# Optimization experiments

Hardware: AMD Instinct MI355X
Metric: run time of the kernel (lower is better)

Reference implementation:

```python
import jax, jax.numpy as jnp
import numpy as np

N_NODES = 100000
DROPOUT_P = 0.2


def _gcn_conv(x, W, b, src, dst, n_nodes):
    # PyG GCNConv: h = x @ W; add self-loops; sym-norm deg^-1/2 aggregation; + bias
    h = x @ W  # [N, D_out]
    loops = jnp.arange(n_nodes, dtype=src.dtype)
    src_all = jnp.concatenate([src, loops])
    dst_all = jnp.concatenate([dst, loops])
    deg = jax.ops.segment_sum(jnp.ones_like(dst_all, dtype=h.dtype), dst_all,
                              num_segments=n_nodes)  # includes self-loops
    dinv = jnp.where(deg > 0, jax.lax.rsqrt(deg), 0.0)
    norm = dinv[src_all] * dinv[dst_all]  # [E+N]
    msg = h[src_all] * norm[:, None]      # gather + scale
    out = jax.ops.segment_sum(msg, dst_all, num_segments=n_nodes)  # scatter-add
    return out + b


def setup_inputs() -> dict:
    key = jax.random.key(0)
    k1, k2, k3, k4 = jax.random.split(key, 4)
    x = jax.random.normal(k1, (N_NODES, 128), dtype=jnp.float32)
    edge_index = jax.random.randint(k2, (2, 1600000), 0, N_NODES, dtype=jnp.int64)
    W1 = jax.random.normal(k3, (128, 64), dtype=jnp.float32) * (1.0 / np.sqrt(128))
    b1 = jnp.zeros((64,), dtype=jnp.float32)
    W2 = jax.random.normal(k4, (64, 32), dtype=jnp.float32) * (1.0 / np.sqrt(64))
    b2 = jnp.zeros((32,), dtype=jnp.float32)
    return {"x": x, "edge_index": edge_index, "W1": W1, "b1": b1, "W2": W2, "b2": b2}


def reference(x, edge_index, W1, b1, W2, b2):
    src, dst = edge_index[0], edge_index[1]
    h1 = _gcn_conv(x, W1, b1, src, dst, N_NODES)
    h1 = jax.nn.relu(h1)
    # F.dropout defaults to training=True -> apply inverted dropout with fixed key
    keep = jax.random.bernoulli(jax.random.key(42), 1.0 - DROPOUT_P, h1.shape)
    h1 = jnp.where(keep, h1 / (1.0 - DROPOUT_P), 0.0)
    h2 = _gcn_conv(h1, W2, b2, src, dst, N_NODES)
    return h2
```

## Files before the change

kernel.cpp:

```cpp
#include <hip/hip_runtime.h>
#include <stdint.h>

#define DIN 128
#define D1 64
#define D2 32
#define MAXDEG 48
#define BCAP 4608
#define CBLK 8192

__device__ __forceinline__ unsigned short f2bf(float v) {
  unsigned u = __float_as_uint(v);
  unsigned r = u + 0x7fffu + ((u >> 16) & 1u);
  return (unsigned short)(r >> 16);
}
__device__ __forceinline__ float bf2f(unsigned short b) {
  return __uint_as_float(((unsigned)b) << 16);
}

__device__ __forceinline__ float node_dinv(const int* __restrict__ deg, int n) {
  return (float)(1.0 / sqrt((double)(deg[n] + 1)));
}

__device__ __forceinline__ unsigned rotl32(unsigned x, int r) {
  return (x << r) | (x >> (32 - r));
}

__device__ __forceinline__ unsigned threefry_fold(unsigned ctr) {
  unsigned k0 = 0u, k1 = 42u;
  unsigned ks0 = k0, ks1 = k1, ks2 = k0 ^ k1 ^ 0x1BD11BDAu;
  unsigned x0 = 0u, x1 = ctr;
  x0 += ks0; x1 += ks1;
#define TF_ROUND(r) { x0 += x1; x1 = rotl32(x1, (r)); x1 ^= x0; }
  TF_ROUND(13) TF_ROUND(15) TF_ROUND(26) TF_ROUND(6)
  x0 += ks1; x1 += ks2 + 1u;
  TF_ROUND(17) TF_ROUND(29) TF_ROUND(16) TF_ROUND(24)
  x0 += ks2; x1 += ks0 + 2u;
  TF_ROUND(13) TF_ROUND(15) TF_ROUND(26) TF_ROUND(6)
  x0 += ks0; x1 += ks1 + 3u;
  TF_ROUND(17) TF_ROUND(29) TF_ROUND(16) TF_ROUND(24)
  x0 += ks1; x1 += ks2 + 4u;
  TF_ROUND(13) TF_ROUND(15) TF_ROUND(26) TF_ROUND(6)
  x0 += ks2; x1 += ks0 + 5u;
#undef TF_ROUND
  return x0 ^ x1;
}

__device__ __forceinline__ float dropout_scale(unsigned idx) {
  unsigned bits = threefry_fold(idx);
  float u = __uint_as_float((bits >> 9) | 0x3f800000u) - 1.0f;
  return (u < 0.8f) ? 1.25f : 0.0f;
}

__global__ __launch_bounds__(256) void bin_kernel(const int* __restrict__ src,
                                                  const int* __restrict__ dst,
                                                  int* __restrict__ cursor,
                                                  uint2* __restrict__ binned,
                                                  int E, int NBK) {
  __shared__ int cnt[512];
  __shared__ int cbase[512];
  const int tid = threadIdx.x;
  const int e0 = blockIdx.x * CBLK;

  for (int b = tid; b < NBK; b += 256) cnt[b] = 0;
  __syncthreads();

#pragma unroll 4
  for (int i = 0; i < CBLK / 256; i++) {
    int e = e0 + tid + 256 * i;
    if (e < E) atomicAdd(&cnt[dst[e] >> 8], 1);
  }
  __syncthreads();

  for (int b = tid; b < NBK; b += 256) {
    int c = cnt[b];
    if (c > 0) cbase[b] = b * BCAP + atomicAdd(&cursor[b], c);
    cnt[b] = 0;
  }
  __syncthreads();

#pragma unroll 4
  for (int i = 0; i < CBLK / 256; i++) {
    int e = e0 + tid + 256 * i;
    if (e < E) {
      int d = dst[e];
      int b = d >> 8;
      int rk = atomicAdd(&cnt[b], 1);
      int pos = cbase[b] + rk;
      if (pos - b * BCAP < BCAP)
        binned[pos] = make_uint2((unsigned)d, (unsigned)src[e]);
    }
  }
}

__global__ __launch_bounds__(256) void ellbuild_kernel(const uint2* __restrict__ binned,
                                                       const int* __restrict__ cursor,
                                                       int* __restrict__ deg,
                                                       int* __restrict__ ell, int N) {
  __shared__ int r[256];
  const int tid = threadIdx.x;
  const int b = blockIdx.x;
  const int nodebase = b << 8;
  r[tid] = 0;
  __syncthreads();

  int cnt = cursor[b];
  if (cnt > BCAP) cnt = BCAP;
  const uint2* seg = binned + (size_t)b * BCAP;
  for (int i = tid; i < cnt; i += 256) {
    uint2 p = seg[i];
    int local = (int)p.x - nodebase;
    int rk = atomicAdd(&r[local], 1);
    if (rk < MAXDEG) ell[(int)p.x * MAXDEG + rk] = (int)p.y;
  }
  __syncthreads();

  int node = nodebase + tid;
  if (node < N) deg[node] = r[tid];
}

__global__ __launch_bounds__(256) void gemm1_kernel(const float* __restrict__ x,
                                                    const float* __restrict__ W1,
                                                    const int* __restrict__ deg,
                                                    unsigned short* __restrict__ h1p, int N) {
  __shared__ float xT[32][65];
  __shared__ float Wl[32][D1];
  const int tid = threadIdx.x;
  const int rowbase = blockIdx.x * 64;
  const int tx = tid & 15;
  const int ty = tid >> 4;
  float acc[4][4];
#pragma unroll
  for (int i = 0; i < 4; i++)
#pragma unroll
    for (int j = 0; j < 4; j++) acc[i][j] = 0.f;

  for (int c4 = 0; c4 < 4; c4++) {
    const int k0 = c4 * 32;
#pragma unroll
    for (int i = 0; i < 2; i++) {
      int f = tid + 256 * i;
      int row = f >> 3;
      int kq = (f & 7) * 4;
      int gr = rowbase + row;
      float4 vv = make_float4(0.f, 0.f, 0.f, 0.f);
      if (gr < N) vv = *(const float4*)(x + (size_t)gr * DIN + k0 + kq);
      xT[kq + 0][row] = vv.x;
      xT[kq + 1][row] = vv.y;
      xT[kq + 2][row] = vv.z;
      xT[kq + 3][row] = vv.w;
    }
#pragma unroll
    for (int i = 0; i < 2; i++) {
      int f = tid + 256 * i;
      int k = f >> 4;
      int cc = (f & 15) * 4;
      *(float4*)&Wl[k][cc] = *(const float4*)(W1 + (size_t)(k0 + k) * D1 + cc);
    }
    __syncthreads();
#pragma unroll 4
    for (int k = 0; k < 32; k++) {
      float4 a = *(const float4*)&xT[k][4 * ty];
      float4 b = *(const float4*)&Wl[k][4 * tx];
      float av[4] = {a.x, a.y, a.z, a.w};
      float bv[4] = {b.x, b.y, b.z, b.w};
#pragma unroll
      for (int i = 0; i < 4; i++)
#pragma unroll
        for (int j = 0; j < 4; j++) acc[i][j] = fmaf(av[i], bv[j], acc[i][j]);
    }
    __syncthreads();
  }

#pragma unroll
  for (int i = 0; i < 4; i++) {
    int gr = rowbase + 4 * ty + i;
    if (gr < N) {
      float di = node_dinv(deg, gr);
      ushort4 o;
      o.x = f2bf(acc[i][0] * di);
      o.y = f2bf(acc[i][1] * di);
      o.z = f2bf(acc[i][2] * di);
      o.w = f2bf(acc[i][3] * di);
      *(ushort4*)(h1p + (size_t)gr * D1 + 4 * tx) = o;
    }
  }
}

__global__ __launch_bounds__(256) void agg1_kernel(const int* __restrict__ deg,
                                                   const int* __restrict__ ell,
                                                   const unsigned short* __restrict__ h1p,
                                                   const float* __restrict__ b1,
                                                   float* __restrict__ h1d, int N) {
  const int wslot = __builtin_amdgcn_readfirstlane(threadIdx.x >> 6);
  const int d = blockIdx.x * 4 + wslot;
  const int f = threadIdx.x & 63;
  const int cnt = min(deg[d], MAXDEG);
  const int base = d * MAXDEG;
  float acc = bf2f(h1p[(size_t)d * D1 + f]);
  int j = 0;
  for (; j + 7 < cnt; j += 8) {
    int s[8];
#pragma unroll
    for (int i = 0; i < 8; i++) s[i] = ell[base + j + i];
    unsigned short a[8];
#pragma unroll
    for (int i = 0; i < 8; i++) a[i] = h1p[(size_t)s[i] * D1 + f];
#pragma unroll
    for (int i = 0; i < 8; i++) acc += bf2f(a[i]);
  }
  for (; j < cnt; ++j) acc += bf2f(h1p[(size_t)ell[base + j] * D1 + f]);
  float di = node_dinv(deg, d);
  float v = fmaf(di, acc, b1[f]);
  v = fmaxf(v, 0.0f);
  v *= dropout_scale((unsigned)(d * D1 + f));
  h1d[(size_t)d * D1 + f] = v;
}

__global__ __launch_bounds__(256) void gemm2_kernel(const float* __restrict__ h1d,
                                                    const float* __restrict__ W2,
                                                    const int* __restrict__ deg,
                                                    unsigned short* __restrict__ h2p, int N) {
  __shared__ float hT[D1][129];
  __shared__ float Wl[D1][D2];
  const int tid = threadIdx.x;
  const int rowbase = blockIdx.x * 128;

#pragma unroll
  for (int i = 0; i < 8; i++) {
    int f = tid + 256 * i;
    int row = f >> 4;
    int kq = (f & 15) * 4;
    int gr = rowbase + row;
    float4 v = make_float4(0.f, 0.f, 0.f, 0.f);
    if (gr < N) v = *(const float4*)(h1d + (size_t)gr * D1 + kq);
    hT[kq + 0][row] = v.x;
    hT[kq + 1][row] = v.y;
    hT[kq + 2][row] = v.z;
    hT[kq + 3][row] = v.w;
  }
#pragma unroll
  for (int i = 0; i < 2; i++) {
    int f = tid + 256 * i;
    int k = f >> 3;
    int c = (f & 7) * 4;
    *(float4*)&Wl[k][c] = *(const float4*)(W2 + (size_t)k * D2 + c);
  }
  __syncthreads();

  const int tx = tid & 7;
  const int ty = tid >> 3;
  float acc[4][4];
#pragma unroll
  for (int i = 0; i < 4; i++)
#pragma unroll
    for (int j = 0; j < 4; j++) acc[i][j] = 0.f;

#pragma unroll 4
  for (int k = 0; k < D1; k++) {
    float4 a = *(const float4*)&hT[k][4 * ty];
    float4 b = *(const float4*)&Wl[k][4 * tx];
    float av[4] = {a.x, a.y, a.z, a.w};
    float bv[4] = {b.x, b.y, b.z, b.w};
#pragma unroll
    for (int i = 0; i < 4; i++)
#pragma unroll
      for (int j = 0; j < 4; j++) acc[i][j] = fmaf(av[i], bv[j], acc[i][j]);
  }

#pragma unroll
  for (int i = 0; i < 4; i++) {
    int gr = rowbase + 4 * ty + i;
    if (gr < N) {
      float di = node_dinv(deg, gr);
      ushort4 o;
      o.x = f2bf(acc[i][0] * di);
      o.y = f2bf(acc[i][1] * di);
      o.z = f2bf(acc[i][2] * di);
      o.w = f2bf(acc[i][3] * di);
      *(ushort4*)(h2p + (size_t)gr * D2 + 4 * tx) = o;
    }
  }
}

__global__ __launch_bounds__(256) void agg2_kernel(const int* __restrict__ deg,
                                                   const int* __restrict__ ell,
                                                   const unsigned short* __restrict__ h2p,
                                                   const float* __restrict__ b2,
                                                   float* __restrict__ out, int N) {
  const int wslot = __builtin_amdgcn_readfirstlane(threadIdx.x >> 6);
  const int d = blockIdx.x * 4 + wslot;
  const int lane = threadIdx.x & 63;
  const int f = lane & 31;
  const int h = lane >> 5;
  const int cnt = min(deg[d], MAXDEG);
  const int base = d * MAXDEG;
  float acc = (h == 0) ? bf2f(h2p[(size_t)d * D2 + f]) : 0.0f;
  int j = h;
  for (; j + 6 < cnt; j += 8) {
    int s0 = ell[base + j], s1 = ell[base + j + 2];
    int s2 = ell[base + j + 4], s3 = ell[base + j + 6];
    unsigned short a0 = h2p[(size_t)s0 * D2 + f];
    unsigned short a1 = h2p[(size_t)s1 * D2 + f];
    unsigned short a2 = h2p[(size_t)s2 * D2 + f];
    unsigned short a3 = h2p[(size_t)s3 * D2 + f];
    acc += bf2f(a0); acc += bf2f(a1); acc += bf2f(a2); acc += bf2f(a3);
  }
  for (; j < cnt; j += 2) acc += bf2f(h2p[(size_t)ell[base + j] * D2 + f]);
  acc += __shfl_down(acc, 32, 64);
  if (h == 0) {
    out[(size_t)d * D2 + f] = fmaf(node_dinv(deg, d), acc, b2[f]);
  }
}

extern "C" void kernel_launch(void* const* d_in, const int* in_sizes, int n_in,
                              void* d_out, int out_size, void* d_ws, size_t ws_size,
                              hipStream_t stream) {
  const float* x  = (const float*)d_in[0];
  const int*   ei = (const int*)d_in[1];
  const float* W1 = (const float*)d_in[2];
  const float* b1 = (const float*)d_in[3];
  const float* W2 = (const float*)d_in[4];
  const float* b2 = (const float*)d_in[5];
  const int N = in_sizes[0] / DIN;
  const int E = in_sizes[1] / 2;
  const int NBK = (N + 255) >> 8;
  const int* src = ei;
  const int* dst = ei + E;
  float* out = (float*)d_out;

  char* ws = (char*)d_ws;
  size_t off = 0;
  auto alloc = [&](size_t bytes) -> char* {
    char* p = ws + off;
    off += (bytes + 255) / 256 * 256;
    return p;
  };
  unsigned short* h1p = (unsigned short*)alloc((size_t)N * D1 * 2);
  float*          h1d = (float*)alloc((size_t)N * D1 * 4);
  int*            ell = (int*)alloc((size_t)N * MAXDEG * 4);
  int*            deg = (int*)alloc((size_t)N * 4);
  int*         cursor = (int*)alloc((size_t)NBK * 4);
  unsigned short* h2p = h1p;
  uint2*       binned = (uint2*)h1d;
  (void)ws_size; (void)n_in; (void)out_size;

  hipMemsetAsync(cursor, 0, (size_t)NBK * 4, stream);

  bin_kernel<<<(E + CBLK - 1) / CBLK, 256, 0, stream>>>(src, dst, cursor, binned, E, NBK);
  ellbuild_kernel<<<NBK, 256, 0, stream>>>(binned, cursor, deg, ell, N);
  gemm1_kernel<<<(N + 63) / 64, 256, 0, stream>>>(x, W1, deg, h1p, N);
  agg1_kernel<<<N / 4, 256, 0, stream>>>(deg, ell, h1p, b1, h1d, N);
  gemm2_kernel<<<(N + 127) / 128, 256, 0, stream>>>(h1d, W2, deg, h2p, N);
  agg2_kernel<<<N / 4, 256, 0, stream>>>(deg, ell, h2p, b2, out, N);
}
```

Baseline: 289.9 us.

## Split feature tables into 16-wide column panels for cache-local gathers

Stores the bf16 h1/h2 and fp32 h1d tables as column panels of 16 features, so each aggregation pass gathers from a smaller footprint that fits better in cache. The aggregation kernels launch one grid slice per panel, with 8 lanes per edge reading 32-bit pairs and 8 edges per wave, then reduce across edges with shuffles. The dropout mask moves into a separate precomputed bitmask kernel. In exchange, the ELL index list is re-read once per panel and the number of blocks grows.

```diff
diff --git a/kernel.cpp b/kernel.cpp
--- a/kernel.cpp
+++ b/kernel.cpp
@@ -4,6 +4,7 @@
 #define DIN 128
 #define D1 64
 #define D2 32
+#define PF 16
 #define MAXDEG 48
 #define BCAP 4608
 #define CBLK 8192
@@ -45,10 +46,14 @@
   return x0 ^ x1;
 }
 
-__device__ __forceinline__ float dropout_scale(unsigned idx) {
-  unsigned bits = threefry_fold(idx);
+__global__ __launch_bounds__(256) void mask_kernel(unsigned long long* __restrict__ mask,
+                                                   int N) {
+  const int d = blockIdx.x * 4 + (threadIdx.x >> 6);
+  const int f = threadIdx.x & 63;
+  unsigned bits = threefry_fold((unsigned)(d * 64 + f));
   float u = __uint_as_float((bits >> 9) | 0x3f800000u) - 1.0f;
-  return (u < 0.8f) ? 1.25f : 0.0f;
+  unsigned long long m = __ballot(u < 0.8f);
+  if (f == 0) mask[d] = m;
 }
 
 __global__ __launch_bounds__(256) void bin_kernel(const int* __restrict__ src,
@@ -181,7 +186,9 @@
       o.y = f2bf(acc[i][1] * di);
       o.z = f2bf(acc[i][2] * di);
       o.w = f2bf(acc[i][3] * di);
-      *(ushort4*)(h1p + (size_t)gr * D1 + 4 * tx) = o;
+      unsigned short* pan = h1p + (size_t)(tx >> 2) * N * PF
+                                + (size_t)gr * PF + ((4 * tx) & 15);
+      *(ushort4*)pan = o;
     }
   }
 }
@@ -190,30 +197,45 @@
                                                    const int* __restrict__ ell,
                                                    const unsigned short* __restrict__ h1p,
                                                    const float* __restrict__ b1,
+                                                   const unsigned long long* __restrict__ mask,
                                                    float* __restrict__ h1d, int N) {
-  const int wslot = __builtin_amdgcn_readfirstlane(threadIdx.x >> 6);
-  const int d = blockIdx.x * 4 + wslot;
-  const int f = threadIdx.x & 63;
+  const int bpp = N / 4;
+  const int p = blockIdx.x / bpp;
+  const int d = (blockIdx.x % bpp) * 4 + (threadIdx.x >> 6);
+  const int lane = threadIdx.x & 63;
+  const int es = lane >> 3;
+  const int dw = lane & 7;
   const int cnt = min(deg[d], MAXDEG);
-  const int base = d * MAXDEG;
-  float acc = bf2f(h1p[(size_t)d * D1 + f]);
-  int j = 0;
-  for (; j + 7 < cnt; j += 8) {
-    int s[8];
-#pragma unroll
-    for (int i = 0; i < 8; i++) s[i] = ell[base + j + i];
-    unsigned short a[8];
-#pragma unroll
-    for (int i = 0; i < 8; i++) a[i] = h1p[(size_t)s[i] * D1 + f];
-#pragma unroll
-    for (int i = 0; i < 8; i++) acc += bf2f(a[i]);
-  }
-  for (; j < cnt; ++j) acc += bf2f(h1p[(size_t)ell[base + j] * D1 + f]);
-  float di = node_dinv(deg, d);
-  float v = fmaf(di, acc, b1[f]);
-  v = fmaxf(v, 0.0f);
-  v *= dropout_scale((unsigned)(d * D1 + f));
-  h1d[(size_t)d * D1 + f] = v;
+  const int ebase = d * MAXDEG;
+  const unsigned* panel = (const unsigned*)h1p + (size_t)p * N * (PF / 2);
+  float ax = 0.f, ay = 0.f;
+  for (int j = 0; j < cnt; j += 8) {
+    if (j + es < cnt) {
+      int s = ell[ebase + j + es];
+      unsigned v = panel[s * 8 + dw];
+      ax += bf2f((unsigned short)(v & 0xffffu));
+      ay += bf2f((unsigned short)(v >> 16));
+    }
+  }
+  ax += __shfl_xor(ax, 8);  ay += __shfl_xor(ay, 8);
+  ax += __shfl_xor(ax, 16); ay += __shfl_xor(ay, 16);
+  ax += __shfl_xor(ax, 32); ay += __shfl_xor(ay, 32);
+  unsigned sv = panel[d * 8 + dw];
+  ax += bf2f((unsigned short)(sv & 0xffffu));
+  ay += bf2f((unsigned short)(sv >> 16));
+  if (es == 0) {
+    float dd = node_dinv(deg, d);
+    int f0 = p * PF + 2 * dw;
+    float2 bb = *(const float2*)(b1 + f0);
+    float vx = fmaf(dd, ax, bb.x);
+    float vy = fmaf(dd, ay, bb.y);
+    vx = fmaxf(vx, 0.f);
+    vy = fmaxf(vy, 0.f);
+    unsigned long long m = mask[d];
+    vx = ((m >> f0) & 1ull) ? vx * 1.25f : 0.f;
+    vy = ((m >> (f0 + 1)) & 1ull) ? vy * 1.25f : 0.f;
+    *(float2*)(h1d + (size_t)p * N * PF + (size_t)d * PF + 2 * dw) = make_float2(vx, vy);
+  }
 }
 
 __global__ __launch_bounds__(256) void gemm2_kernel(const float* __restrict__ h1d,
@@ -232,7 +254,8 @@
     int kq = (f & 15) * 4;
     int gr = rowbase + row;
     float4 v = make_float4(0.f, 0.f, 0.f, 0.f);
-    if (gr < N) v = *(const float4*)(h1d + (size_t)gr * D1 + kq);
+    if (gr < N)
+      v = *(const float4*)(h1d + (size_t)(kq >> 4) * N * PF + (size_t)gr * PF + (kq & 15));
     hT[kq + 0][row] = v.x;
     hT[kq + 1][row] = v.y;
     hT[kq + 2][row] = v.z;
@@ -277,7 +300,9 @@
       o.y = f2bf(acc[i][1] * di);
       o.z = f2bf(acc[i][2] * di);
       o.w = f2bf(acc[i][3] * di);
-      *(ushort4*)(h2p + (size_t)gr * D2 + 4 * tx) = o;
+      unsigned short* pan = h2p + (size_t)(tx >> 2) * N * PF
+                                + (size_t)gr * PF + ((4 * tx) & 15);
+      *(ushort4*)pan = o;
     }
   }
 }
@@ -287,28 +312,37 @@
                                                    const unsigned short* __restrict__ h2p,
                                                    const float* __restrict__ b2,
                                                    float* __restrict__ out, int N) {
-  const int wslot = __builtin_amdgcn_readfirstlane(threadIdx.x >> 6);
-  const int d = blockIdx.x * 4 + wslot;
+  const int bpp = N / 4;
+  const int p = blockIdx.x / bpp;
+  const int d = (blockIdx.x % bpp) * 4 + (threadIdx.x >> 6);
   const int lane = threadIdx.x & 63;
-  const int f = lane & 31;
-  const int h = lane >> 5;
+  const int es = lane >> 3;
+  const int dw = lane & 7;
   const int cnt = min(deg[d], MAXDEG);
-  const int base = d * MAXDEG;
-  float acc = (h == 0) ? bf2f(h2p[(size_t)d * D2 + f]) : 0.0f;
-  int j = h;
-  for (; j + 6 < cnt; j += 8) {
-    int s0 = ell[base + j], s1 = ell[base + j + 2];
-    int s2 = ell[base + j + 4], s3 = ell[base + j + 6];
-    unsigned short a0 = h2p[(size_t)s0 * D2 + f];
-    unsigned short a1 = h2p[(size_t)s1 * D2 + f];
-    unsigned short a2 = h2p[(size_t)s2 * D2 + f];
-    unsigned short a3 = h2p[(size_t)s3 * D2 + f];
-    acc += bf2f(a0); acc += bf2f(a1); acc += bf2f(a2); acc += bf2f(a3);
-  }
-  for (; j < cnt; j += 2) acc += bf2f(h2p[(size_t)ell[base + j] * D2 + f]);
-  acc += __shfl_down(acc, 32, 64);
-  if (h == 0) {
-    out[(size_t)d * D2 + f] = fmaf(node_dinv(deg, d), acc, b2[f]);
+  const int ebase = d * MAXDEG;
+  const unsigned* panel = (const unsigned*)h2p + (size_t)p * N * (PF / 2);
+  float ax = 0.f, ay = 0.f;
+  for (int j = 0; j < cnt; j += 8) {
+    if (j + es < cnt) {
+      int s = ell[ebase + j + es];
+      unsigned v = panel[s * 8 + dw];
+      ax += bf2f((unsigned short)(v & 0xffffu));
+      ay += bf2f((unsigned short)(v >> 16));
+    }
+  }
+  ax += __shfl_xor(ax, 8);  ay += __shfl_xor(ay, 8);
+  ax += __shfl_xor(ax, 16); ay += __shfl_xor(ay, 16);
+  ax += __shfl_xor(ax, 32); ay += __shfl_xor(ay, 32);
+  unsigned sv = panel[d * 8 + dw];
+  ax += bf2f((unsigned short)(sv & 0xffffu));
+  ay += bf2f((unsigned short)(sv >> 16));
+  if (es == 0) {
+    float dd = node_dinv(deg, d);
+    int f0 = p * PF + 2 * dw;
+    float2 bb = *(const float2*)(b2 + f0);
+    float vx = fmaf(dd, ax, bb.x);
+    float vy = fmaf(dd, ay, bb.y);
+    *(float2*)(out + (size_t)d * D2 + f0) = make_float2(vx, vy);
   }
 }
 
@@ -339,6 +373,7 @@
   float*          h1d = (float*)alloc((size_t)N * D1 * 4);
   int*            ell = (int*)alloc((size_t)N * MAXDEG * 4);
   int*            deg = (int*)alloc((size_t)N * 4);
+  unsigned long long* mask = (unsigned long long*)alloc((size_t)N * 8);
   int*         cursor = (int*)alloc((size_t)NBK * 4);
   unsigned short* h2p = h1p;
   uint2*       binned = (uint2*)h1d;
@@ -346,10 +381,11 @@
 
   hipMemsetAsync(cursor, 0, (size_t)NBK * 4, stream);
 
+  mask_kernel<<<N / 4, 256, 0, stream>>>(mask, N);
   bin_kernel<<<(E + CBLK - 1) / CBLK, 256, 0, stream>>>(src, dst, cursor, binned, E, NBK);
   ellbuild_kernel<<<NBK, 256, 0, stream>>>(binned, cursor, deg, ell, N);
   gemm1_kernel<<<(N + 63) / 64, 256, 0, stream>>>(x, W1, deg, h1p, N);
-  agg1_kernel<<<N / 4, 256, 0, stream>>>(deg, ell, h1p, b1, h1d, N);
+  agg1_kernel<<<(N / 4) * 4, 256, 0, stream>>>(deg, ell, h1p, b1, mask, h1d, N);
   gemm2_kernel<<<(N + 127) / 128, 256, 0, stream>>>(h1d, W2, deg, h2p, N);
-  agg2_kernel<<<N / 4, 256, 0, stream>>>(deg, ell, h2p, b2, out, N);
-}
+  agg2_kernel<<<(N / 4) * 2, 256, 0, stream>>>(deg, ell, h2p, b2, out, N);
+}
```

Result: slower. 422.4 us (+45.7%).
